# Optimization experiments

Measured on AMD Instinct MI355X. Metric: run time of the kernel, lower is better.

## Reference

```python
import jax, jax.numpy as jnp
import numpy as np

B, N, D_IN, D_OUT, MAX_POS = 256, 256, 768, 300, 256
NEG_INF = -9e15
LEAKY_SLOPE = 0.2


def setup_inputs() -> dict:
    key = jax.random.key(0)
    ks = jax.random.split(key, 6)
    h = jax.random.normal(ks[0], (B, N, D_IN), dtype=jnp.float32)
    adj = (jax.random.uniform(ks[1], (B, N, N)) > 0.9).astype(jnp.float32)
    adj = jnp.maximum(adj, jnp.eye(N, dtype=jnp.float32)[None])
    positions = jax.random.randint(ks[2], (B, N), 0, MAX_POS)
    W = jax.random.normal(ks[3], (D_IN, D_OUT), dtype=jnp.float32) * (1.0 / np.sqrt(D_IN))
    a_src = jax.random.normal(ks[4], (1, D_OUT), dtype=jnp.float32) * 0.05
    a_dst = jax.random.normal(ks[5], (1, D_OUT), dtype=jnp.float32) * 0.05
    pos_table = jax.random.normal(jax.random.fold_in(key, 7), (MAX_POS, D_OUT), dtype=jnp.float32)
    return {"h": h, "adj": adj, "positions": positions, "W": W,
            "a_src": a_src, "a_dst": a_dst, "pos_table": pos_table}


def reference(h, adj, positions, W, a_src, a_dst, pos_table):
    # Wh = W(h) + position embedding          [B, N, D_OUT]
    Wh = jnp.einsum('bni,io->bno', h, W) + pos_table[positions]
    # additive attention scores
    f_src = jnp.einsum('bno,o->bn', Wh, a_src[0])  # [B, N]
    f_dst = jnp.einsum('bno,o->bn', Wh, a_dst[0])  # [B, N]
    e = f_src[:, :, None] + f_dst[:, None, :]      # [B, N, N]
    e = jnp.where(e >= 0, e, LEAKY_SLOPE * e)      # LeakyReLU(0.2)
    # adjacency masking + softmax over last dim
    masked = jnp.where(adj > 0, e, NEG_INF)
    attention = jax.nn.softmax(masked, axis=-1)
    # (eval mode: edge dropout and dropout are identity)
    h_prime = jnp.einsum('bnm,bmo->bno', attention, Wh)
    return h_prime, attention
```

## Files before the change

kernel.cpp:

```cpp
#include <hip/hip_runtime.h>

#define B_    256
#define N_    256
#define DIN   768
#define DOUT  300
#define DOUTP 320
#define NT    20
#define M_    (B_*N_)
#define HP_ELEMS (M_*DOUT)
#define NEG_INF -9.0e15f

typedef _Float16 f16;
typedef __attribute__((ext_vector_type(8))) _Float16 f16x8;
typedef __attribute__((ext_vector_type(4))) _Float16 f16x4;
typedef __attribute__((ext_vector_type(4))) float    f32x4;

__device__ __forceinline__ void async_copy16(void* lds, const void* g) {
    __builtin_amdgcn_global_load_lds(
        (const __attribute__((address_space(1))) void*)g,
        (__attribute__((address_space(3))) void*)lds, 16, 0, 0);
}

__global__ __launch_bounds__(256) void prep_wt(const float* __restrict__ W,
                                               f16* __restrict__ Wt) {
    int idx = blockIdx.x * 256 + threadIdx.x;
    if (idx >= DOUTP * DIN) return;
    int n = idx / DIN, k = idx - n * DIN;
    float v = (n < DOUT) ? W[k * DOUT + n] : 0.0f;
    Wt[idx] = (f16)v;
}

__global__ __launch_bounds__(256, 3) void gemm1(
    const float* __restrict__ h, const f16* __restrict__ Wt,
    const int* __restrict__ positions,
    const float* __restrict__ a_src, const float* __restrict__ a_dst,
    const float* __restrict__ pos_table,
    f16* __restrict__ WhT, float* __restrict__ f_src, float* __restrict__ f_dst)
{
    __shared__ f16 Al[64 * 40];
    __shared__ f16 Bl[DOUTP * 32];
    __shared__ float pfs[64][2], pfd[64][2];

    const int tid  = threadIdx.x;
    const int wave = tid >> 6, lane = tid & 63;
    const int quad = lane >> 4, c = lane & 15;
    const int rh = wave & 1;
    const int chf = wave >> 1;
    const int rowbase = blockIdx.x * 64;

    const int brow = lane >> 2;
    const int bj   = (lane & 3) ^ (brow & 3);

    const int ar = tid >> 2, aj = tid & 3;

    f32x4 acc[2][10];
#pragma unroll
    for (int rt = 0; rt < 2; ++rt)
#pragma unroll
        for (int i = 0; i < 10; ++i) acc[rt][i] = (f32x4){0.f, 0.f, 0.f, 0.f};

    for (int kt = 0; kt < DIN / 32; ++kt) {
#pragma unroll
        for (int i = 0; i < 5; ++i) {
            int chk = wave + 4 * i;
            int n = chk * 16 + brow;
            async_copy16((char*)Bl + chk * 1024,
                         Wt + (size_t)n * DIN + kt * 32 + bj * 8);
        }
        {
            const float4* src = (const float4*)(h + (size_t)(rowbase + ar) * DIN + kt * 32 + aj * 8);
            float4 v0 = src[0], v1 = src[1];
            *(f16x8*)&Al[ar * 40 + aj * 8] =
                (f16x8){(f16)v0.x, (f16)v0.y, (f16)v0.z, (f16)v0.w,
                        (f16)v1.x, (f16)v1.y, (f16)v1.z, (f16)v1.w};
        }
        __syncthreads();

        f16x8 af0 = *(const f16x8*)&Al[(rh * 32 + c) * 40 + quad * 8];
        f16x8 af1 = *(const f16x8*)&Al[(rh * 32 + 16 + c) * 40 + quad * 8];
#pragma unroll
        for (int i = 0; i < 10; ++i) {
            int n = (chf * 10 + i) * 16 + c;
            f16x8 bf = *(const f16x8*)&Bl[n * 32 + (quad ^ (n & 3)) * 8];
            acc[0][i] = __builtin_amdgcn_mfma_f32_16x16x32_f16(af0, bf, acc[0][i], 0, 0, 0);
            acc[1][i] = __builtin_amdgcn_mfma_f32_16x16x32_f16(af1, bf, acc[1][i], 0, 0, 0);
        }
        __syncthreads();
    }

    const int bidx  = rowbase >> 8;
    const int mloc  = (rowbase & 255);

    int posr[2][4];
#pragma unroll
    for (int rt = 0; rt < 2; ++rt)
#pragma unroll
        for (int r = 0; r < 4; ++r)
            posr[rt][r] = positions[rowbase + rh * 32 + rt * 16 + quad * 4 + r];

    float fs[2][4] = {{0,0,0,0},{0,0,0,0}}, fd[2][4] = {{0,0,0,0},{0,0,0,0}};
#pragma unroll
    for (int i = 0; i < 10; ++i) {
        int col = (chf * 10 + i) * 16 + c;
        if (col < DOUT) {
            float as = a_src[col], ad = a_dst[col];
#pragma unroll
            for (int rt = 0; rt < 2; ++rt)
#pragma unroll
                for (int r = 0; r < 4; ++r) {
                    float v = acc[rt][i][r] + pos_table[posr[rt][r] * DOUT + col];
                    acc[rt][i][r] = v;
                    fs[rt][r] += v * as;
                    fd[rt][r] += v * ad;
                }
        } else {
#pragma unroll
            for (int rt = 0; rt < 2; ++rt)
#pragma unroll
                for (int r = 0; r < 4; ++r) acc[rt][i][r] = 0.0f;
        }
    }
#pragma unroll
    for (int off = 1; off < 16; off <<= 1) {
#pragma unroll
        for (int rt = 0; rt < 2; ++rt)
#pragma unroll
            for (int r = 0; r < 4; ++r) {
                fs[rt][r] += __shfl_xor(fs[rt][r], off, 16);
                fd[rt][r] += __shfl_xor(fd[rt][r], off, 16);
            }
    }
    if (c == 0) {
#pragma unroll
        for (int rt = 0; rt < 2; ++rt)
#pragma unroll
            for (int r = 0; r < 4; ++r) {
                int row = rh * 32 + rt * 16 + quad * 4 + r;
                pfs[row][chf] = fs[rt][r];
                pfd[row][chf] = fd[rt][r];
            }
    }
#pragma unroll
    for (int i = 0; i < 10; ++i) {
        int col = (chf * 10 + i) * 16 + c;
#pragma unroll
        for (int rt = 0; rt < 2; ++rt) {
            int mrow = mloc + rh * 32 + rt * 16 + quad * 4;
            f16x4 u = (f16x4){(f16)acc[rt][i][0], (f16)acc[rt][i][1],
                              (f16)acc[rt][i][2], (f16)acc[rt][i][3]};
            *(f16x4*)(WhT + ((size_t)bidx * DOUTP + col) * N_ + mrow) = u;
        }
    }
    __syncthreads();
    if (tid < 64) {
        f_src[rowbase + tid] = pfs[tid][0] + pfs[tid][1];
        f_dst[rowbase + tid] = pfd[tid][0] + pfd[tid][1];
    }
}

__global__ __launch_bounds__(256) void softmax_att(
    const float* __restrict__ adj, const float* __restrict__ f_src,
    const float* __restrict__ f_dst, float* __restrict__ att)
{
    const int wave = threadIdx.x >> 6, lane = threadIdx.x & 63;
    const int row = blockIdx.x * 4 + wave;
    const int b = row >> 8;

    float fs = f_src[row];
    float4 fd4 = *(const float4*)(f_dst + b * N_ + lane * 4);
    float4 a4  = *(const float4*)(adj + (size_t)row * N_ + lane * 4);

    float e[4];
    {
        float v;
        v = fs + fd4.x; v = v >= 0.f ? v : 0.2f * v; e[0] = a4.x > 0.f ? v : NEG_INF;
        v = fs + fd4.y; v = v >= 0.f ? v : 0.2f * v; e[1] = a4.y > 0.f ? v : NEG_INF;
        v = fs + fd4.z; v = v >= 0.f ? v : 0.2f * v; e[2] = a4.z > 0.f ? v : NEG_INF;
        v = fs + fd4.w; v = v >= 0.f ? v : 0.2f * v; e[3] = a4.w > 0.f ? v : NEG_INF;
    }
    float mx = fmaxf(fmaxf(e[0], e[1]), fmaxf(e[2], e[3]));
#pragma unroll
    for (int off = 1; off < 64; off <<= 1) mx = fmaxf(mx, __shfl_xor(mx, off, 64));

    float p[4], s = 0.f;
#pragma unroll
    for (int i = 0; i < 4; ++i) { p[i] = __expf(e[i] - mx); s += p[i]; }
#pragma unroll
    for (int off = 1; off < 64; off <<= 1) s += __shfl_xor(s, off, 64);

    float inv = 1.0f / s;
    *(float4*)(att + (size_t)row * N_ + lane * 4) =
        make_float4(p[0] * inv, p[1] * inv, p[2] * inv, p[3] * inv);
}

__global__ __launch_bounds__(256, 3) void gemm2(
    const float* __restrict__ att, const f16* __restrict__ WhT,
    float* __restrict__ hp)
{
    __shared__ f16 Al[64 * 40];
    __shared__ f16 Bl[DOUTP * 32];

    const int tid  = threadIdx.x;
    const int wave = tid >> 6, lane = tid & 63;
    const int quad = lane >> 4, c = lane & 15;
    const int rh = wave & 1;
    const int chf = wave >> 1;
    const int rowbase = blockIdx.x * 64;
    const int bidx = rowbase >> 8;

    const int brow = lane >> 2;
    const int bj   = (lane & 3) ^ (brow & 3);
    const int ar = tid >> 2, aj = tid & 3;

    f32x4 acc[2][10];
#pragma unroll
    for (int rt = 0; rt < 2; ++rt)
#pragma unroll
        for (int i = 0; i < 10; ++i) acc[rt][i] = (f32x4){0.f, 0.f, 0.f, 0.f};

    for (int kt = 0; kt < N_ / 32; ++kt) {
#pragma unroll
        for (int i = 0; i < 5; ++i) {
            int chk = wave + 4 * i;
            int n = chk * 16 + brow;
            async_copy16((char*)Bl + chk * 1024,
                         WhT + ((size_t)bidx * DOUTP + n) * N_ + kt * 32 + bj * 8);
        }
        {
            const float4* src = (const float4*)(att + (size_t)(rowbase + ar) * N_ + kt * 32 + aj * 8);
            float4 v0 = src[0], v1 = src[1];
            *(f16x8*)&Al[ar * 40 + aj * 8] =
                (f16x8){(f16)v0.x, (f16)v0.y, (f16)v0.z, (f16)v0.w,
                        (f16)v1.x, (f16)v1.y, (f16)v1.z, (f16)v1.w};
        }
        __syncthreads();

        f16x8 af0 = *(const f16x8*)&Al[(rh * 32 + c) * 40 + quad * 8];
        f16x8 af1 = *(const f16x8*)&Al[(rh * 32 + 16 + c) * 40 + quad * 8];
#pragma unroll
        for (int i = 0; i < 10; ++i) {
            int n = (chf * 10 + i) * 16 + c;
            f16x8 bf = *(const f16x8*)&Bl[n * 32 + (quad ^ (n & 3)) * 8];
            acc[0][i] = __builtin_amdgcn_mfma_f32_16x16x32_f16(af0, bf, acc[0][i], 0, 0, 0);
            acc[1][i] = __builtin_amdgcn_mfma_f32_16x16x32_f16(af1, bf, acc[1][i], 0, 0, 0);
        }
        __syncthreads();
    }

#pragma unroll
    for (int i = 0; i < 10; ++i) {
        int col = (chf * 10 + i) * 16 + c;
        if (col < DOUT) {
#pragma unroll
            for (int rt = 0; rt < 2; ++rt) {
                int row0 = rowbase + rh * 32 + rt * 16 + quad * 4;
#pragma unroll
                for (int r = 0; r < 4; ++r)
                    hp[(size_t)(row0 + r) * DOUT + col] = acc[rt][i][r];
            }
        }
    }
}

extern "C" void kernel_launch(void* const* d_in, const int* in_sizes, int n_in,
                              void* d_out, int out_size, void* d_ws, size_t ws_size,
                              hipStream_t stream)
{
    const float* h         = (const float*)d_in[0];
    const float* adj       = (const float*)d_in[1];
    const int*   positions = (const int*)d_in[2];
    const float* W         = (const float*)d_in[3];
    const float* a_src     = (const float*)d_in[4];
    const float* a_dst     = (const float*)d_in[5];
    const float* pos_table = (const float*)d_in[6];

    float* hp  = (float*)d_out;
    float* att = hp + HP_ELEMS;

    f16*   Wt    = (f16*)d_ws;
    f16*   WhT   = Wt + (size_t)DOUTP * DIN;
    float* f_src = (float*)(WhT + (size_t)B_ * DOUTP * N_);
    float* f_dst = f_src + M_;

    hipLaunchKernelGGL(prep_wt,     dim3((DOUTP * DIN + 255) / 256), dim3(256), 0, stream, W, Wt);
    hipLaunchKernelGGL(gemm1,       dim3(M_ / 64),  dim3(256), 0, stream,
                       h, Wt, positions, a_src, a_dst, pos_table, WhT, f_src, f_dst);
    hipLaunchKernelGGL(softmax_att, dim3(M_ / 4),   dim3(256), 0, stream, adj, f_src, f_dst, att);
    hipLaunchKernelGGL(gemm2,       dim3(M_ / 64),  dim3(256), 0, stream, att, WhT, hp);
}
```

Baseline: 469.9 us.

## Fuse softmax into second GEMM and retile first GEMM with pre-swizzled layouts

The softmax kernel is merged into the second GEMM. Attention probabilities are written to global memory once and also kept as f16 in shared memory, so the fp32 attention matrix no longer has to be read back. W and Wh are stored in k-tiled, pre-swizzled layouts so each tile loads as one contiguous async copy, and the B-operand loads in the fused kernel are double-buffered. The first GEMM now uses 32-row tiles and stages each half of the h row block in shared memory, trading more LDS and lower occupancy for fewer loads and fewer barriers.

```diff
diff --git a/kernel.cpp b/kernel.cpp
--- a/kernel.cpp
+++ b/kernel.cpp
@@ -5,7 +5,6 @@
 #define DIN   768
 #define DOUT  300
 #define DOUTP 320
-#define NT    20
 #define M_    (B_*N_)
 #define HP_ELEMS (M_*DOUT)
 #define NEG_INF -9.0e15f
@@ -22,86 +21,108 @@
 }
 
 __global__ __launch_bounds__(256) void prep_wt(const float* __restrict__ W,
-                                               f16* __restrict__ Wt) {
+                                               f16* __restrict__ WtT) {
     int idx = blockIdx.x * 256 + threadIdx.x;
-    if (idx >= DOUTP * DIN) return;
-    int n = idx / DIN, k = idx - n * DIN;
+    if (idx >= DIN * DOUTP) return;
+    int k = idx / DOUTP, n = idx - k * DOUTP;
     float v = (n < DOUT) ? W[k * DOUT + n] : 0.0f;
-    Wt[idx] = (f16)v;
+    int kt = k >> 5, sl = ((k >> 3) & 3) ^ ((n >> 1) & 3), e = k & 7;
+    WtT[(((size_t)kt * DOUTP + n) << 5) + (sl << 3) + e] = (f16)v;
 }
 
 __global__ __launch_bounds__(256, 3) void gemm1(
-    const float* __restrict__ h, const f16* __restrict__ Wt,
+    const float* __restrict__ h, const f16* __restrict__ WtT,
     const int* __restrict__ positions,
     const float* __restrict__ a_src, const float* __restrict__ a_dst,
     const float* __restrict__ pos_table,
-    f16* __restrict__ WhT, float* __restrict__ f_src, float* __restrict__ f_dst)
+    f16* __restrict__ WhT2, float* __restrict__ f_src, float* __restrict__ f_dst)
 {
-    __shared__ f16 Al[64 * 40];
-    __shared__ f16 Bl[DOUTP * 32];
-    __shared__ float pfs[64][2], pfd[64][2];
+    __shared__ f16 Ah[32 * 384];
+    __shared__ f16 Bs[DOUTP * 32];
+    __shared__ float pfs[32][4], pfd[32][4];
 
     const int tid  = threadIdx.x;
     const int wave = tid >> 6, lane = tid & 63;
     const int quad = lane >> 4, c = lane & 15;
-    const int rh = wave & 1;
-    const int chf = wave >> 1;
-    const int rowbase = blockIdx.x * 64;
-
-    const int brow = lane >> 2;
-    const int bj   = (lane & 3) ^ (brow & 3);
-
-    const int ar = tid >> 2, aj = tid & 3;
-
-    f32x4 acc[2][10];
+    const int rowbase = blockIdx.x * 32;
+
+    const int crow = tid >> 3, cl8 = tid & 7;
+    const float* cbase = h + (size_t)(rowbase + crow) * DIN;
+
+    int boff[5];
+#pragma unroll
+    for (int i = 0; i < 5; ++i) {
+        int n = (wave * 5 + i) * 16 + c;
+        boff[i] = n * 32 + ((quad ^ ((n >> 1) & 3)) << 3);
+    }
+    const int arow0 = c * 384, arow1 = (16 + c) * 384;
+    const int cx7 = c & 7;
+
+    f32x4 acc[2][5];
 #pragma unroll
     for (int rt = 0; rt < 2; ++rt)
 #pragma unroll
-        for (int i = 0; i < 10; ++i) acc[rt][i] = (f32x4){0.f, 0.f, 0.f, 0.f};
-
-    for (int kt = 0; kt < DIN / 32; ++kt) {
-#pragma unroll
-        for (int i = 0; i < 5; ++i) {
-            int chk = wave + 4 * i;
-            int n = chk * 16 + brow;
-            async_copy16((char*)Bl + chk * 1024,
-                         Wt + (size_t)n * DIN + kt * 32 + bj * 8);
-        }
-        {
-            const float4* src = (const float4*)(h + (size_t)(rowbase + ar) * DIN + kt * 32 + aj * 8);
-            float4 v0 = src[0], v1 = src[1];
-            *(f16x8*)&Al[ar * 40 + aj * 8] =
+        for (int i = 0; i < 5; ++i) acc[rt][i] = (f32x4){0.f, 0.f, 0.f, 0.f};
+
+    for (int half = 0; half < 2; ++half) {
+#pragma unroll
+        for (int j = 0; j < 6; ++j) {
+            int c8 = j * 8 + cl8;
+            const float4* s = (const float4*)(cbase + half * 384 + c8 * 8);
+            float4 v0 = s[0], v1 = s[1];
+            int slot = c8 ^ (crow & 7);
+            *(f16x8*)&Ah[crow * 384 + slot * 8] =
                 (f16x8){(f16)v0.x, (f16)v0.y, (f16)v0.z, (f16)v0.w,
                         (f16)v1.x, (f16)v1.y, (f16)v1.z, (f16)v1.w};
         }
         __syncthreads();
 
-        f16x8 af0 = *(const f16x8*)&Al[(rh * 32 + c) * 40 + quad * 8];
-        f16x8 af1 = *(const f16x8*)&Al[(rh * 32 + 16 + c) * 40 + quad * 8];
-#pragma unroll
-        for (int i = 0; i < 10; ++i) {
-            int n = (chf * 10 + i) * 16 + c;
-            f16x8 bf = *(const f16x8*)&Bl[n * 32 + (quad ^ (n & 3)) * 8];
-            acc[0][i] = __builtin_amdgcn_mfma_f32_16x16x32_f16(af0, bf, acc[0][i], 0, 0, 0);
-            acc[1][i] = __builtin_amdgcn_mfma_f32_16x16x32_f16(af1, bf, acc[1][i], 0, 0, 0);
-        }
-        __syncthreads();
-    }
-
-    const int bidx  = rowbase >> 8;
-    const int mloc  = (rowbase & 255);
+#pragma unroll
+        for (int kt12 = 0; kt12 < 12; ++kt12) {
+            const int kt = half * 12 + kt12;
+#pragma unroll
+            for (int i = 0; i < 5; ++i) {
+                int chk = wave * 5 + i;
+                async_copy16((char*)Bs + chk * 1024,
+                             (const char*)WtT + (size_t)kt * 20480 + chk * 1024 + lane * 16);
+            }
+            __builtin_amdgcn_sched_barrier(0);
+            asm volatile("s_waitcnt vmcnt(0)");
+            __builtin_amdgcn_sched_barrier(0);
+            __builtin_amdgcn_s_barrier();
+            __builtin_amdgcn_sched_barrier(0);
+
+            int k4 = kt12 * 4 + quad;
+            f16x8 af0 = *(const f16x8*)&Ah[arow0 + ((k4 ^ cx7) << 3)];
+            f16x8 af1 = *(const f16x8*)&Ah[arow1 + ((k4 ^ cx7) << 3)];
+            __builtin_amdgcn_s_setprio(1);
+#pragma unroll
+            for (int i = 0; i < 5; ++i) {
+                f16x8 bf = *(const f16x8*)&Bs[boff[i]];
+                acc[0][i] = __builtin_amdgcn_mfma_f32_16x16x32_f16(af0, bf, acc[0][i], 0, 0, 0);
+                acc[1][i] = __builtin_amdgcn_mfma_f32_16x16x32_f16(af1, bf, acc[1][i], 0, 0, 0);
+            }
+            __builtin_amdgcn_s_setprio(0);
+            __builtin_amdgcn_sched_barrier(0);
+            __builtin_amdgcn_s_barrier();
+            __builtin_amdgcn_sched_barrier(0);
+        }
+    }
+
+    const int bidx = rowbase >> 8;
+    const int ktb  = (rowbase & 255) >> 5;
 
     int posr[2][4];
 #pragma unroll
     for (int rt = 0; rt < 2; ++rt)
 #pragma unroll
         for (int r = 0; r < 4; ++r)
-            posr[rt][r] = positions[rowbase + rh * 32 + rt * 16 + quad * 4 + r];
+            posr[rt][r] = positions[rowbase + rt * 16 + quad * 4 + r];
 
     float fs[2][4] = {{0,0,0,0},{0,0,0,0}}, fd[2][4] = {{0,0,0,0},{0,0,0,0}};
 #pragma unroll
-    for (int i = 0; i < 10; ++i) {
-        int col = (chf * 10 + i) * 16 + c;
+    for (int i = 0; i < 5; ++i) {
+        int col = (wave * 5 + i) * 16 + c;
         if (col < DOUT) {
             float as = a_src[col], ad = a_dst[col];
 #pragma unroll
@@ -135,70 +156,37 @@
         for (int rt = 0; rt < 2; ++rt)
 #pragma unroll
             for (int r = 0; r < 4; ++r) {
-                int row = rh * 32 + rt * 16 + quad * 4 + r;
-                pfs[row][chf] = fs[rt][r];
-                pfd[row][chf] = fd[rt][r];
-            }
-    }
-#pragma unroll
-    for (int i = 0; i < 10; ++i) {
-        int col = (chf * 10 + i) * 16 + c;
+                int row = rt * 16 + quad * 4 + r;
+                pfs[row][wave] = fs[rt][r];
+                pfd[row][wave] = fd[rt][r];
+            }
+    }
+#pragma unroll
+    for (int i = 0; i < 5; ++i) {
+        int col = (wave * 5 + i) * 16 + c;
 #pragma unroll
         for (int rt = 0; rt < 2; ++rt) {
-            int mrow = mloc + rh * 32 + rt * 16 + quad * 4;
             f16x4 u = (f16x4){(f16)acc[rt][i][0], (f16)acc[rt][i][1],
                               (f16)acc[rt][i][2], (f16)acc[rt][i][3]};
-            *(f16x4*)(WhT + ((size_t)bidx * DOUTP + col) * N_ + mrow) = u;
+            int sl = (rt * 2 + (quad >> 1)) ^ ((col >> 1) & 3);
+            *(f16x4*)(WhT2 + (((size_t)(bidx * 8 + ktb) * DOUTP + col) << 5)
+                           + (sl << 3) + ((quad & 1) << 2)) = u;
         }
     }
     __syncthreads();
-    if (tid < 64) {
-        f_src[rowbase + tid] = pfs[tid][0] + pfs[tid][1];
-        f_dst[rowbase + tid] = pfd[tid][0] + pfd[tid][1];
-    }
-}
-
-__global__ __launch_bounds__(256) void softmax_att(
+    if (tid < 32) {
+        f_src[rowbase + tid] = pfs[tid][0] + pfs[tid][1] + pfs[tid][2] + pfs[tid][3];
+        f_dst[rowbase + tid] = pfd[tid][0] + pfd[tid][1] + pfd[tid][2] + pfd[tid][3];
+    }
+}
+
+__global__ __launch_bounds__(256, 2) void fused2(
     const float* __restrict__ adj, const float* __restrict__ f_src,
-    const float* __restrict__ f_dst, float* __restrict__ att)
+    const float* __restrict__ f_dst, const f16* __restrict__ WhT2,
+    float* __restrict__ att, float* __restrict__ hp)
 {
-    const int wave = threadIdx.x >> 6, lane = threadIdx.x & 63;
-    const int row = blockIdx.x * 4 + wave;
-    const int b = row >> 8;
-
-    float fs = f_src[row];
-    float4 fd4 = *(const float4*)(f_dst + b * N_ + lane * 4);
-    float4 a4  = *(const float4*)(adj + (size_t)row * N_ + lane * 4);
-
-    float e[4];
-    {
-        float v;
-        v = fs + fd4.x; v = v >= 0.f ? v : 0.2f * v; e[0] = a4.x > 0.f ? v : NEG_INF;
-        v = fs + fd4.y; v = v >= 0.f ? v : 0.2f * v; e[1] = a4.y > 0.f ? v : NEG_INF;
-        v = fs + fd4.z; v = v >= 0.f ? v : 0.2f * v; e[2] = a4.z > 0.f ? v : NEG_INF;
-        v = fs + fd4.w; v = v >= 0.f ? v : 0.2f * v; e[3] = a4.w > 0.f ? v : NEG_INF;
-    }
-    float mx = fmaxf(fmaxf(e[0], e[1]), fmaxf(e[2], e[3]));
-#pragma unroll
-    for (int off = 1; off < 64; off <<= 1) mx = fmaxf(mx, __shfl_xor(mx, off, 64));
-
-    float p[4], s = 0.f;
-#pragma unroll
-    for (int i = 0; i < 4; ++i) { p[i] = __expf(e[i] - mx); s += p[i]; }
-#pragma unroll
-    for (int off = 1; off < 64; off <<= 1) s += __shfl_xor(s, off, 64);
-
-    float inv = 1.0f / s;
-    *(float4*)(att + (size_t)row * N_ + lane * 4) =
-        make_float4(p[0] * inv, p[1] * inv, p[2] * inv, p[3] * inv);
-}
-
-__global__ __launch_bounds__(256, 3) void gemm2(
-    const float* __restrict__ att, const f16* __restrict__ WhT,
-    float* __restrict__ hp)
-{
-    __shared__ f16 Al[64 * 40];
-    __shared__ f16 Bl[DOUTP * 32];
+    __shared__ f16 Pl[64 * 256];
+    __shared__ f16 Bl[2][DOUTP * 32];
 
     const int tid  = threadIdx.x;
     const int wave = tid >> 6, lane = tid & 63;
@@ -208,9 +196,56 @@
     const int rowbase = blockIdx.x * 64;
     const int bidx = rowbase >> 8;
 
-    const int brow = lane >> 2;
-    const int bj   = (lane & 3) ^ (brow & 3);
-    const int ar = tid >> 2, aj = tid & 3;
+#define STAGE_B2(K, BUF) do {                                                  \
+    _Pragma("unroll")                                                          \
+    for (int i_ = 0; i_ < 5; ++i_) {                                           \
+        int chk_ = wave * 5 + i_;                                              \
+        async_copy16((char*)Bl[(BUF)] + chk_ * 1024,                           \
+                     (const char*)WhT2 + (size_t)(bidx * 8 + (K)) * 20480      \
+                                       + chk_ * 1024 + lane * 16);             \
+    } } while (0)
+
+    STAGE_B2(0, 0);
+    STAGE_B2(1, 1);
+
+    {
+        float4 fd4 = *(const float4*)(f_dst + bidx * N_ + lane * 4);
+        const float* arow = adj + (size_t)(rowbase + wave * 16) * N_ + lane * 4;
+        float4 nx0 = *(const float4*)arow;
+        float4 nx1 = *(const float4*)(arow + N_);
+        for (int rr = 0; rr < 16; ++rr) {
+            float4 a4 = nx0;
+            nx0 = nx1;
+            if (rr + 2 < 16) nx1 = *(const float4*)(arow + (size_t)(rr + 2) * N_);
+            const int lrow = wave * 16 + rr;
+            const int row  = rowbase + lrow;
+            float fsv = f_src[row];
+
+            float v, e0, e1, e2, e3;
+            v = fsv + fd4.x; v = v >= 0.f ? v : 0.2f * v; e0 = a4.x > 0.f ? v : NEG_INF;
+            v = fsv + fd4.y; v = v >= 0.f ? v : 0.2f * v; e1 = a4.y > 0.f ? v : NEG_INF;
+            v = fsv + fd4.z; v = v >= 0.f ? v : 0.2f * v; e2 = a4.z > 0.f ? v : NEG_INF;
+            v = fsv + fd4.w; v = v >= 0.f ? v : 0.2f * v; e3 = a4.w > 0.f ? v : NEG_INF;
+
+            float mx = fmaxf(fmaxf(e0, e1), fmaxf(e2, e3));
+#pragma unroll
+            for (int off = 1; off < 64; off <<= 1) mx = fmaxf(mx, __shfl_xor(mx, off, 64));
+
+            float p0 = __expf(e0 - mx), p1 = __expf(e1 - mx);
+            float p2 = __expf(e2 - mx), p3 = __expf(e3 - mx);
+            float s = p0 + p1 + p2 + p3;
+#pragma unroll
+            for (int off = 1; off < 64; off <<= 1) s += __shfl_xor(s, off, 64);
+
+            float inv = 1.0f / s;
+            *(float4*)(att + (size_t)row * N_ + lane * 4) =
+                make_float4(p0 * inv, p1 * inv, p2 * inv, p3 * inv);
+            int slot = (lane >> 1) ^ (lrow & 7);
+            *(f16x4*)&Pl[lrow * 256 + slot * 8 + (lane & 1) * 4] =
+                (f16x4){(f16)(p0 * inv), (f16)(p1 * inv), (f16)(p2 * inv), (f16)(p3 * inv)};
+        }
+    }
+    __syncthreads();
 
     f32x4 acc[2][10];
 #pragma unroll
@@ -218,34 +253,41 @@
 #pragma unroll
         for (int i = 0; i < 10; ++i) acc[rt][i] = (f32x4){0.f, 0.f, 0.f, 0.f};
 
-    for (int kt = 0; kt < N_ / 32; ++kt) {
-#pragma unroll
-        for (int i = 0; i < 5; ++i) {
-            int chk = wave + 4 * i;
-            int n = chk * 16 + brow;
-            async_copy16((char*)Bl + chk * 1024,
-                         WhT + ((size_t)bidx * DOUTP + n) * N_ + kt * 32 + bj * 8);
-        }
-        {
-            const float4* src = (const float4*)(att + (size_t)(rowbase + ar) * N_ + kt * 32 + aj * 8);
-            float4 v0 = src[0], v1 = src[1];
-            *(f16x8*)&Al[ar * 40 + aj * 8] =
-                (f16x8){(f16)v0.x, (f16)v0.y, (f16)v0.z, (f16)v0.w,
-                        (f16)v1.x, (f16)v1.y, (f16)v1.z, (f16)v1.w};
-        }
-        __syncthreads();
-
-        f16x8 af0 = *(const f16x8*)&Al[(rh * 32 + c) * 40 + quad * 8];
-        f16x8 af1 = *(const f16x8*)&Al[(rh * 32 + 16 + c) * 40 + quad * 8];
+    const int ar0 = (rh * 32 + c) * 256, ar1 = (rh * 32 + 16 + c) * 256;
+    const int cx7 = c & 7;
+
+#pragma unroll
+    for (int kt = 0; kt < 8; ++kt) {
+        int k4 = kt * 4 + quad;
+        f16x8 af0 = *(const f16x8*)&Pl[ar0 + ((k4 ^ cx7) << 3)];
+        f16x8 af1 = *(const f16x8*)&Pl[ar1 + ((k4 ^ cx7) << 3)];
+        __builtin_amdgcn_s_setprio(1);
 #pragma unroll
         for (int i = 0; i < 10; ++i) {
             int n = (chf * 10 + i) * 16 + c;
-            f16x8 bf = *(const f16x8*)&Bl[n * 32 + (quad ^ (n & 3)) * 8];
+            f16x8 bf = *(const f16x8*)&Bl[kt & 1][n * 32 + ((quad ^ ((n >> 1) & 3)) << 3)];
             acc[0][i] = __builtin_amdgcn_mfma_f32_16x16x32_f16(af0, bf, acc[0][i], 0, 0, 0);
             acc[1][i] = __builtin_amdgcn_mfma_f32_16x16x32_f16(af1, bf, acc[1][i], 0, 0, 0);
         }
-        __syncthreads();
-    }
+        __builtin_amdgcn_s_setprio(0);
+        if (kt < 7) {
+            __builtin_amdgcn_sched_barrier(0);
+            __builtin_amdgcn_s_barrier();
+            __builtin_amdgcn_sched_barrier(0);
+            if (kt + 2 < 8) {
+                STAGE_B2(kt + 2, kt & 1);
+                __builtin_amdgcn_sched_barrier(0);
+                asm volatile("s_waitcnt vmcnt(5)");
+            } else {
+                __builtin_amdgcn_sched_barrier(0);
+                asm volatile("s_waitcnt vmcnt(0)");
+            }
+            __builtin_amdgcn_sched_barrier(0);
+            __builtin_amdgcn_s_barrier();
+            __builtin_amdgcn_sched_barrier(0);
+        }
+    }
+#undef STAGE_B2
 
 #pragma unroll
     for (int i = 0; i < 10; ++i) {
@@ -277,14 +319,14 @@
     float* hp  = (float*)d_out;
     float* att = hp + HP_ELEMS;
 
-    f16*   Wt    = (f16*)d_ws;
-    f16*   WhT   = Wt + (size_t)DOUTP * DIN;
-    float* f_src = (float*)(WhT + (size_t)B_ * DOUTP * N_);
+    f16*   WtT   = (f16*)d_ws;
+    f16*   WhT2  = WtT + (size_t)DOUTP * DIN;
+    float* f_src = (float*)(WhT2 + (size_t)B_ * DOUTP * N_);
     float* f_dst = f_src + M_;
 
-    hipLaunchKernelGGL(prep_wt,     dim3((DOUTP * DIN + 255) / 256), dim3(256), 0, stream, W, Wt);
-    hipLaunchKernelGGL(gemm1,       dim3(M_ / 64),  dim3(256), 0, stream,
-                       h, Wt, positions, a_src, a_dst, pos_table, WhT, f_src, f_dst);
-    hipLaunchKernelGGL(softmax_att, dim3(M_ / 4),   dim3(256), 0, stream, adj, f_src, f_dst, att);
-    hipLaunchKernelGGL(gemm2,       dim3(M_ / 64),  dim3(256), 0, stream, att, WhT, hp);
-}
+    hipLaunchKernelGGL(prep_wt, dim3((DIN * DOUTP + 255) / 256), dim3(256), 0, stream, W, WtT);
+    hipLaunchKernelGGL(gemm1,   dim3(M_ / 32), dim3(256), 0, stream,
+                       h, WtT, positions, a_src, a_dst, pos_table, WhT2, f_src, f_dst);
+    hipLaunchKernelGGL(fused2,  dim3(M_ / 64), dim3(256), 0, stream,
+                       adj, f_src, f_dst, WhT2, att, hp);
+}
```

Measured after the change: 455.7 us. 3.0% less time.
